# Kernel tuning notes

Hardware: AMD Instinct MI355X
Metric: run time of the kernel (lower is better)

The kernel has to match this reference:

```python
import jax, jax.numpy as jnp
import numpy as np

B, T, NH, EX, VOCAB, NLAYER = 8, 510, 12, 768, 256, 6
NBLK = 2 * NLAYER - 1          # 11 blocks, all with out=ex
NE = T + 2                     # CustomEmb output dim = n_embd = 512
HD = EX // NH
EXIT_SCALE = 1.0 / float(np.sqrt(4 * NBLK))  # torch init divides 'exit' params by sqrt(#exit params)


def _ln(x, s, b):
    m = jnp.mean(x, axis=-1, keepdims=True)
    v = jnp.mean((x - m) ** 2, axis=-1, keepdims=True)
    return (x - m) * jax.lax.rsqrt(v + 1e-5) * s + b


def setup_inputs() -> dict:
    key = jax.random.key(0)
    ks = iter(jax.random.split(key, 40))
    def n(shape, scale=0.02):
        return jax.random.normal(next(ks), shape, jnp.float32) * scale
    inp = {}
    inp['idx'] = jax.random.randint(next(ks), (B, T), 0, 2)
    inp['lin_w'] = n((NE, EX)); inp['lin_b'] = n((EX,))
    # stacked per-block params (leading dim NBLK), torch Linear math y = x @ W + b with W stored (in,out)
    inp['ln1_s'] = jnp.ones((NBLK, EX), jnp.float32); inp['ln1_b'] = jnp.zeros((NBLK, EX), jnp.float32)
    inp['qw'] = n((NBLK, EX, EX)); inp['qb'] = n((NBLK, EX))
    inp['kw'] = n((NBLK, EX, EX)); inp['kb'] = n((NBLK, EX))
    inp['vw'] = n((NBLK, EX, EX)); inp['vb'] = n((NBLK, EX))
    inp['ew'] = n((NBLK, EX, EX)) * EXIT_SCALE; inp['eb'] = n((NBLK, EX)) * EXIT_SCALE
    inp['ln2_s'] = jnp.ones((NBLK, EX), jnp.float32); inp['ln2_b'] = jnp.zeros((NBLK, EX), jnp.float32)
    inp['m1w'] = n((NBLK, EX, 4 * EX)); inp['m1b'] = n((NBLK, 4 * EX))
    inp['m2w'] = n((NBLK, 4 * EX, EX)) * EXIT_SCALE; inp['m2b'] = n((NBLK, EX)) * EXIT_SCALE
    inp['lnf_s'] = jnp.ones((EX,), jnp.float32); inp['lnf_b'] = jnp.zeros((EX,), jnp.float32)
    inp['head_w'] = n((EX * T, VOCAB)); inp['head_b'] = n((VOCAB,))
    return inp


def reference(idx, lin_w, lin_b, ln1_s, ln1_b, qw, qb, kw, kb, vw, vb, ew, eb,
              ln2_s, ln2_b, m1w, m1b, m2w, m2b, lnf_s, lnf_b, head_w, head_b):
    # CustomEmb: one-hot of binary token + identity positional encoding -> [B,T,T+2]
    e0 = (idx == 0).astype(jnp.float32)
    e1 = (idx == 1).astype(jnp.float32)
    pos = jnp.broadcast_to(jnp.eye(T, dtype=jnp.float32), (B, T, T))
    x = jnp.concatenate([e0[:, :, None], e1[:, :, None], pos], axis=2)
    x = jax.nn.relu(x @ lin_w + lin_b)                       # [B,T,EX]
    mask = jnp.tril(jnp.ones((T, T), bool))
    inv_sqrt_d = 1.0 / float(np.sqrt(HD))

    def block(x, p):
        l1s, l1b, Qw, Qb, Kw, Kb, Vw, Vb, Ew, Eb, l2s, l2b, M1w, M1b, M2w, M2b = p
        h = _ln(x, l1s, l1b)
        q = (h @ Qw + Qb).reshape(B, T, NH, HD)
        k = (h @ Kw + Kb).reshape(B, T, NH, HD)
        v = (h @ Vw + Vb).reshape(B, T, NH, HD)
        att = jnp.einsum('bqhd,bkhd->bhqk', q, k) * inv_sqrt_d
        att = jnp.where(mask, att, -jnp.inf)
        probs = jax.nn.softmax(att, axis=-1)
        y = jnp.einsum('bhqk,bkhd->bqhd', probs, v).reshape(B, T, EX)
        x = x + y @ Ew + Eb
        h2 = _ln(x, l2s, l2b)
        x = x + jax.nn.relu(h2 @ M1w + M1b) @ M2w + M2b      # MLP depth=2: initial+relu+exit
        return x, None

    x, _ = jax.lax.scan(block, x, (ln1_s, ln1_b, qw, qb, kw, kb, vw, vb,
                                   ew, eb, ln2_s, ln2_b, m1w, m1b, m2w, m2b))
    x = _ln(x, lnf_s, lnf_b)
    return x.reshape(B, -1) @ head_w + head_b                # [B, VOCAB]
```

## Files before the change

### kernel.cpp

```cpp
#include <hip/hip_runtime.h>
#include <hip/hip_bf16.h>
#include <math.h>

constexpr int cB = 8, cT = 510, cNH = 12, cEX = 768, cVOC = 256, cNBLK = 11, cHD = 64;
constexpr int cMB = 512;
constexpr int cMP = 4096;
constexpr int cQKV = 3 * cEX;

typedef __attribute__((ext_vector_type(8))) short bf16x8;
typedef __attribute__((ext_vector_type(4))) float f32x4;
using bf16 = __hip_bfloat16;

__device__ inline void gload16(const void* g, void* l) {
    __builtin_amdgcn_global_load_lds((const __attribute__((address_space(1))) unsigned int*)g,
                                     (__attribute__((address_space(3))) unsigned int*)l, 16, 0, 0);
}
__device__ inline short f2bs(float f) {
    bf16 b = __float2bfloat16(f);
    return *reinterpret_cast<short*>(&b);
}
__device__ inline float bs2f(unsigned short s) {
    unsigned int u = ((unsigned int)s) << 16;
    float f;
    __builtin_memcpy(&f, &u, 4);
    return f;
}

__global__ __launch_bounds__(256) void embed_kernel(
    const int* __restrict__ idx, const float* __restrict__ lin_w,
    const float* __restrict__ lin_b, short* __restrict__ x)
{
    int row = blockIdx.x;
    int b = row >> 9, t = row & 511;
    short* xr = x + (size_t)row * cEX;
    if (t >= cT) {
        for (int j = threadIdx.x; j < cEX; j += 256) xr[j] = 0;
        return;
    }
    int tok = idx[b * cT + t] & 1;
    const float* wt = lin_w + (size_t)tok * cEX;
    const float* wp = lin_w + (size_t)(2 + t) * cEX;
    for (int j = threadIdx.x; j < cEX; j += 256) {
        float val = wt[j] + wp[j] + lin_b[j];
        xr[j] = f2bs(fmaxf(val, 0.0f));
    }
}

__global__ __launch_bounds__(256) void ln_wave(
    const short* __restrict__ in, const float* __restrict__ s,
    const float* __restrict__ bsh, short* __restrict__ out)
{
    const int wid = threadIdx.x >> 6, lane = threadIdx.x & 63;
    const int row = blockIdx.x * 4 + wid;
    const short* xr = in + (size_t)row * cEX;
    float v[12];
    float sum = 0.f, sq = 0.f;
#pragma unroll
    for (int p = 0; p < 3; ++p) {
        ushort4 raw = *(const ushort4*)&xr[p * 256 + lane * 4];
        v[p * 4 + 0] = bs2f(raw.x); v[p * 4 + 1] = bs2f(raw.y);
        v[p * 4 + 2] = bs2f(raw.z); v[p * 4 + 3] = bs2f(raw.w);
#pragma unroll
        for (int q = 0; q < 4; ++q) { sum += v[p * 4 + q]; sq += v[p * 4 + q] * v[p * 4 + q]; }
    }
#pragma unroll
    for (int off = 1; off < 64; off <<= 1) {
        sum += __shfl_xor(sum, off, 64);
        sq  += __shfl_xor(sq, off, 64);
    }
    float mean = sum * (1.0f / cEX);
    float var = sq * (1.0f / cEX) - mean * mean;
    float rstd = rsqrtf(var + 1e-5f);
    short* outr = out + (size_t)row * cEX;
#pragma unroll
    for (int p = 0; p < 3; ++p) {
        int c = p * 256 + lane * 4;
        float4 sv = *(const float4*)&s[c];
        float4 bv = *(const float4*)&bsh[c];
        short4 pk;
        pk.x = f2bs((v[p * 4 + 0] - mean) * rstd * sv.x + bv.x);
        pk.y = f2bs((v[p * 4 + 1] - mean) * rstd * sv.y + bv.y);
        pk.z = f2bs((v[p * 4 + 2] - mean) * rstd * sv.z + bv.z);
        pk.w = f2bs((v[p * 4 + 3] - mean) * rstd * sv.w + bv.w);
        *(short4*)&outr[c] = pk;
    }
}

__global__ __launch_bounds__(256) void transpose_w(
    const float* __restrict__ W, bf16* __restrict__ WT,
    int K, int N, size_t w_stride, size_t wt_stride, int wt_row_off)
{
    __shared__ float t[32][33];
    const float* Wb = W + (size_t)blockIdx.z * w_stride;
    bf16* WTb = WT + (size_t)blockIdx.z * wt_stride;
    int n0 = blockIdx.x * 32, k0 = blockIdx.y * 32;
    int c = threadIdx.x & 31, ty = threadIdx.x >> 5;
#pragma unroll
    for (int it = 0; it < 4; ++it) {
        int r = ty + it * 8;
        t[r][c] = Wb[(size_t)(k0 + r) * N + n0 + c];
    }
    __syncthreads();
#pragma unroll
    for (int it = 0; it < 4; ++it) {
        int a = ty + it * 8;
        WTb[(size_t)(wt_row_off + n0 + a) * K + k0 + c] = __float2bfloat16(t[c][a]);
    }
}

__global__ __launch_bounds__(256) void transpose_qkv(
    const float* __restrict__ qw, const float* __restrict__ kw,
    const float* __restrict__ vw, bf16* __restrict__ WT)
{
    __shared__ float t[32][33];
    int z = blockIdx.z;
    int blk = z / 3, which = z - blk * 3;
    const float* Wb = (which == 0 ? qw : which == 1 ? kw : vw) + (size_t)blk * cEX * cEX;
    bf16* WTb = WT + (size_t)blk * cQKV * cEX + (size_t)which * cEX * cEX;
    int n0 = blockIdx.x * 32, k0 = blockIdx.y * 32;
    int c = threadIdx.x & 31, ty = threadIdx.x >> 5;
#pragma unroll
    for (int it = 0; it < 4; ++it) {
        int r = ty + it * 8;
        t[r][c] = Wb[(size_t)(k0 + r) * cEX + n0 + c];
    }
    __syncthreads();
#pragma unroll
    for (int it = 0; it < 4; ++it) {
        int a = ty + it * 8;
        WTb[(size_t)(n0 + a) * cEX + k0 + c] = __float2bfloat16(t[c][a]);
    }
}

__global__ __launch_bounds__(256) void concat_bias(
    const float* __restrict__ qb, const float* __restrict__ kb,
    const float* __restrict__ vb, float* __restrict__ qkvb)
{
    int i = blockIdx.x * 256 + threadIdx.x;
    if (i >= cNBLK * cQKV) return;
    int blk = i / cQKV, c = i - blk * cQKV;
    const float* src; int cc = c;
    if (c < cEX)            { src = qb; }
    else if (c < 2 * cEX)   { src = kb; cc = c - cEX; }
    else                    { src = vb; cc = c - 2 * cEX; }
    qkvb[i] = src[(size_t)blk * cEX + cc];
}

template<int FM, int FN, bool RELU, bool RESID, bool OUTBF16, bool VT>
__global__ __launch_bounds__(256) void gemm_db(
    const short* __restrict__ A, const short* __restrict__ BT,
    const float* __restrict__ bias, const short* __restrict__ resid,
    void* __restrict__ Cout, short* __restrict__ vTr, int K, int N)
{
    constexpr int BM = FM * 32, BN = FN * 32;
    constexpr int TS = (BM + BN) * 64;
    constexpr int CA = BM / 32, CB = BN / 32;
    constexpr int LPT = CA + CB;
    static_assert(LPT >= 5 && LPT <= 8, "vmcnt literal range");
    __shared__ short lds[2 * TS];
    const int tid = threadIdx.x;
    const int lane = tid & 63, wid = tid >> 6;
    const int wm = wid >> 1, wn = wid & 1;
    const int bm = blockIdx.y * BM, bn = blockIdx.x * BN;
    const int li = lane & 15, gk = lane >> 4;

    f32x4 acc[FM][FN];
#pragma unroll
    for (int i = 0; i < FM; ++i)
#pragma unroll
        for (int j = 0; j < FN; ++j)
            acc[i][j] = f32x4{0.f, 0.f, 0.f, 0.f};

    auto stage = [&](int kt, int buf) {
        short* la = &lds[buf * TS];
        short* lb = la + BM * 64;
#pragma unroll
        for (int i = 0; i < CA; ++i) {
            int s = i * 256 + tid;
            int r = s >> 3, c = s & 7;
            gload16(A + (size_t)(bm + r) * K + kt * 64 + (c ^ (r & 7)) * 8,
                    (char*)la + (size_t)(i * 256 + wid * 64) * 16);
        }
#pragma unroll
        for (int i = 0; i < CB; ++i) {
            int s = i * 256 + tid;
            int r = s >> 3, c = s & 7;
            gload16(BT + (size_t)(bn + r) * K + kt * 64 + (c ^ (r & 7)) * 8,
                    (char*)lb + (size_t)(i * 256 + wid * 64) * 16);
        }
    };

    const int nkt = K >> 6;
    stage(0, 0);
    stage(1, 1);

    for (int t = 0; t < nkt; ++t) {
        if (t + 1 < nkt) {
            if constexpr (LPT == 5)      asm volatile("s_waitcnt vmcnt(5)" ::: "memory");
            else if constexpr (LPT == 6) asm volatile("s_waitcnt vmcnt(6)" ::: "memory");
            else if constexpr (LPT == 7) asm volatile("s_waitcnt vmcnt(7)" ::: "memory");
            else                         asm volatile("s_waitcnt vmcnt(8)" ::: "memory");
        } else {
            asm volatile("s_waitcnt vmcnt(0)" ::: "memory");
        }
        __builtin_amdgcn_s_barrier();

        const short* la = &lds[(t & 1) * TS];
        const short* lb = la + BM * 64;

        bf16x8 af0[FM], bf0[FN];
#pragma unroll
        for (int mi = 0; mi < FM; ++mi) {
            int row = (wm * FM + mi) * 16 + li;
            af0[mi] = *(const bf16x8*)&la[row * 64 + (gk ^ (row & 7)) * 8];
        }
#pragma unroll
        for (int ni = 0; ni < FN; ++ni) {
            int row = (wn * FN + ni) * 16 + li;
            bf0[ni] = *(const bf16x8*)&lb[row * 64 + (gk ^ (row & 7)) * 8];
        }
        __builtin_amdgcn_s_setprio(1);
#pragma unroll
        for (int mi = 0; mi < FM; ++mi)
#pragma unroll
            for (int ni = 0; ni < FN; ++ni)
                acc[mi][ni] = __builtin_amdgcn_mfma_f32_16x16x32_bf16(
                    af0[mi], bf0[ni], acc[mi][ni], 0, 0, 0);
        __builtin_amdgcn_s_setprio(0);

        bf16x8 af1[FM], bf1[FN];
#pragma unroll
        for (int mi = 0; mi < FM; ++mi) {
            int row = (wm * FM + mi) * 16 + li;
            af1[mi] = *(const bf16x8*)&la[row * 64 + ((4 + gk) ^ (row & 7)) * 8];
        }
#pragma unroll
        for (int ni = 0; ni < FN; ++ni) {
            int row = (wn * FN + ni) * 16 + li;
            bf1[ni] = *(const bf16x8*)&lb[row * 64 + ((4 + gk) ^ (row & 7)) * 8];
        }
        asm volatile("s_waitcnt lgkmcnt(0)" ::: "memory");
        __builtin_amdgcn_s_barrier();
        if (t + 2 < nkt) stage(t + 2, t & 1);
        __builtin_amdgcn_s_setprio(1);
#pragma unroll
        for (int mi = 0; mi < FM; ++mi)
#pragma unroll
            for (int ni = 0; ni < FN; ++ni)
                acc[mi][ni] = __builtin_amdgcn_mfma_f32_16x16x32_bf16(
                    af1[mi], bf1[ni], acc[mi][ni], 0, 0, 0);
        __builtin_amdgcn_s_setprio(0);
    }

#pragma unroll
    for (int mi = 0; mi < FM; ++mi) {
#pragma unroll
        for (int ni = 0; ni < FN; ++ni) {
            int col = bn + (wn * FN + ni) * 16 + li;
            float bv = bias[col];
            int row0 = bm + (wm * FM + mi) * 16 + gk * 4;
            if (VT && col >= 2 * cEX) {
                short4 pk;
                pk.x = f2bs(acc[mi][ni][0] + bv);
                pk.y = f2bs(acc[mi][ni][1] + bv);
                pk.z = f2bs(acc[mi][ni][2] + bv);
                pk.w = f2bs(acc[mi][ni][3] + bv);
                *(short4*)&vTr[(size_t)(col - 2 * cEX) * cMP + row0] = pk;
            } else {
#pragma unroll
                for (int j = 0; j < 4; ++j) {
                    int row = row0 + j;
                    float v = acc[mi][ni][j] + bv;
                    if (RELU) v = fmaxf(v, 0.0f);
                    if (RESID) v += bs2f((unsigned short)resid[(size_t)row * N + col]);
                    if (OUTBF16)
                        ((bf16*)Cout)[(size_t)row * N + col] = __float2bfloat16(v);
                    else
                        ((float*)Cout)[(size_t)row * N + col] = v;
                }
            }
        }
    }
}

__global__ __launch_bounds__(256) void attn_mfma(
    const short* __restrict__ qkv, const short* __restrict__ vT, bf16* __restrict__ y)
{
    const int bid = blockIdx.x;
    const int q8 = bid & 7;
    const int j = bid >> 3;
    const int rng = bid >> 8;
    int qt;
    if (rng == 0)      qt = q8;
    else if (rng == 1) qt = 7 - q8;
    else               qt = (q8 + j) & 7;
    const int h = j % cNH, b = j / cNH;

    __shared__ short Ks[2][64 * 64];
    __shared__ short Vs[2][64 * 64];
    __shared__ short Ss[4][16][72];
    const int tid = threadIdx.x;
    const int lane = tid & 63, wid = tid >> 6;
    const int li = lane & 15, gk = lane >> 4;

    const size_t rowb = (size_t)b * cMB;
    int qr = qt * 64 + wid * 16 + li;
    int qrc = qr < cT ? qr : cT - 1;
    const short* qrow = qkv + (rowb + qrc) * cQKV + h * cHD;
    bf16x8 qf0 = *(const bf16x8*)(qrow + gk * 8);
    bf16x8 qf1 = *(const bf16x8*)(qrow + 32 + gk * 8);

    f32x4 o[4];
    float mrow[4], lrow[4];
#pragma unroll
    for (int dt = 0; dt < 4; ++dt) o[dt] = f32x4{0.f, 0.f, 0.f, 0.f};
#pragma unroll
    for (int jj = 0; jj < 4; ++jj) { mrow[jj] = -3e38f; lrow[jj] = 0.f; }

    const int qloc = qt * 64 + wid * 16 + gk * 4;

    auto stage = [&](int kt, int buf) {
#pragma unroll
        for (int i = 0; i < 2; ++i) {
            int s = i * 256 + tid;
            int r = s >> 3, c = s & 7;
            gload16(qkv + (rowb + kt * 64 + r) * cQKV + cEX + h * cHD + (c ^ (r & 7)) * 8,
                    (char*)&Ks[buf][0] + (size_t)(i * 256 + wid * 64) * 16);
        }
#pragma unroll
        for (int i = 0; i < 2; ++i) {
            int s = i * 256 + tid;
            int d = s >> 3, c = s & 7;
            gload16(vT + (size_t)(h * cHD + d) * cMP + rowb + kt * 64 + (c ^ (d & 7)) * 8,
                    (char*)&Vs[buf][0] + (size_t)(i * 256 + wid * 64) * 16);
        }
    };

    const int nkt = qt + 1;
    stage(0, 0);
    for (int kt = 0; kt < nkt; ++kt) {
        if (kt + 1 < nkt) {
            stage(kt + 1, (kt + 1) & 1);
            asm volatile("s_waitcnt vmcnt(4)" ::: "memory");
        } else {
            asm volatile("s_waitcnt vmcnt(0)" ::: "memory");
        }
        __builtin_amdgcn_s_barrier();
        const int cur = kt & 1;

        f32x4 sg[4];
#pragma unroll
        for (int g = 0; g < 4; ++g) sg[g] = f32x4{0.f, 0.f, 0.f, 0.f};
        __builtin_amdgcn_s_setprio(1);
#pragma unroll
        for (int g = 0; g < 4; ++g) {
            int key = g * 16 + li;
            bf16x8 k0 = *(const bf16x8*)&Ks[cur][key * 64 + (gk ^ (key & 7)) * 8];
            bf16x8 k1 = *(const bf16x8*)&Ks[cur][key * 64 + ((4 + gk) ^ (key & 7)) * 8];
            sg[g] = __builtin_amdgcn_mfma_f32_16x16x32_bf16(qf0, k0, sg[g], 0, 0, 0);
            sg[g] = __builtin_amdgcn_mfma_f32_16x16x32_bf16(qf1, k1, sg[g], 0, 0, 0);
        }
        __builtin_amdgcn_s_setprio(0);

#pragma unroll
        for (int jj = 0; jj < 4; ++jj) {
            int q = qloc + jj;
            float sc[4];
#pragma unroll
            for (int g = 0; g < 4; ++g) {
                int kg = kt * 64 + g * 16 + li;
                sc[g] = (kg <= q) ? sg[g][jj] * 0.125f : -3e38f;
            }
            float tm = fmaxf(fmaxf(sc[0], sc[1]), fmaxf(sc[2], sc[3]));
            tm = fmaxf(tm, __shfl_xor(tm, 1, 16));
            tm = fmaxf(tm, __shfl_xor(tm, 2, 16));
            tm = fmaxf(tm, __shfl_xor(tm, 4, 16));
            tm = fmaxf(tm, __shfl_xor(tm, 8, 16));
            float mnew = fmaxf(mrow[jj], tm);
            float p[4], ps = 0.f;
#pragma unroll
            for (int g = 0; g < 4; ++g) { p[g] = __expf(sc[g] - mnew); ps += p[g]; }
            ps += __shfl_xor(ps, 1, 16);
            ps += __shfl_xor(ps, 2, 16);
            ps += __shfl_xor(ps, 4, 16);
            ps += __shfl_xor(ps, 8, 16);
            float scale = __expf(mrow[jj] - mnew);
            lrow[jj] = lrow[jj] * scale + ps;
            mrow[jj] = mnew;
#pragma unroll
            for (int dt = 0; dt < 4; ++dt) o[dt][jj] *= scale;
#pragma unroll
            for (int g = 0; g < 4; ++g)
                Ss[wid][gk * 4 + jj][g * 16 + li] = f2bs(p[g]);
        }

        bf16x8 pa0 = *(const bf16x8*)&Ss[wid][li][gk * 8];
        bf16x8 pa1 = *(const bf16x8*)&Ss[wid][li][32 + gk * 8];
        __builtin_amdgcn_s_setprio(1);
#pragma unroll
        for (int dt = 0; dt < 4; ++dt) {
            int d = dt * 16 + li;
            bf16x8 vf0 = *(const bf16x8*)&Vs[cur][d * 64 + (gk ^ (d & 7)) * 8];
            bf16x8 vf1 = *(const bf16x8*)&Vs[cur][d * 64 + ((4 + gk) ^ (d & 7)) * 8];
            o[dt] = __builtin_amdgcn_mfma_f32_16x16x32_bf16(pa0, vf0, o[dt], 0, 0, 0);
            o[dt] = __builtin_amdgcn_mfma_f32_16x16x32_bf16(pa1, vf1, o[dt], 0, 0, 0);
        }
        __builtin_amdgcn_s_setprio(0);
        asm volatile("s_waitcnt lgkmcnt(0)" ::: "memory");
        __builtin_amdgcn_s_barrier();
    }

#pragma unroll
    for (int jj = 0; jj < 4; ++jj) {
        int q = qloc + jj;
        if (q >= cT) continue;
        float inv = 1.0f / lrow[jj];
        bf16* yr = y + (rowb + q) * cEX + h * cHD;
#pragma unroll
        for (int dt = 0; dt < 4; ++dt)
            yr[dt * 16 + li] = __float2bfloat16(o[dt][jj] * inv);
    }
}

__global__ __launch_bounds__(256) void head_part_kernel(
    const short* __restrict__ x, const float* __restrict__ lnf_s,
    const float* __restrict__ lnf_b, const float* __restrict__ hw,
    float* __restrict__ part)
{
    __shared__ float xs[8][1536];
    __shared__ float stat[16][2];
    const int tid = threadIdx.x;
    const int trow0 = blockIdx.x * 2;
    const int wid = tid >> 6, lane = tid & 63;
    {
        const int g = lane >> 4, li = lane & 15;
        const int p = wid * 4 + g, bb = p >> 1, rr = p & 1;
        const short* xr = x + ((size_t)(bb * cMB + trow0 + rr)) * cEX;
        float sum = 0.f, sq = 0.f;
#pragma unroll
        for (int it = 0; it < 12; ++it) {
            ushort4 raw = *(const ushort4*)&xr[it * 64 + li * 4];
            float a0 = bs2f(raw.x), a1 = bs2f(raw.y), a2 = bs2f(raw.z), a3 = bs2f(raw.w);
            sum += a0 + a1 + a2 + a3;
            sq  += a0 * a0 + a1 * a1 + a2 * a2 + a3 * a3;
        }
#pragma unroll
        for (int off = 8; off > 0; off >>= 1) {
            sum += __shfl_xor(sum, off, 16);
            sq  += __shfl_xor(sq, off, 16);
        }
        if (li == 0) {
            float mean = sum * (1.0f / cEX);
            float var = sq * (1.0f / cEX) - mean * mean;
            stat[p][0] = mean;
            stat[p][1] = rsqrtf(var + 1e-5f);
        }
    }
    __syncthreads();
    for (int i = tid; i < 8 * 1536; i += 256) {
        int bb = i / 1536, kk = i - bb * 1536;
        int rr = kk >= cEX ? 1 : 0;
        int e = kk - rr * cEX;
        float mean = stat[bb * 2 + rr][0], rstd = stat[bb * 2 + rr][1];
        float val = bs2f((unsigned short)x[((size_t)(bb * cMB + trow0 + rr)) * cEX + e]);
        xs[bb][kk] = (val - mean) * rstd * lnf_s[e] + lnf_b[e];
    }
    __syncthreads();
    float acc[8] = {};
    const int k0 = blockIdx.x * 1536;
    const float* wp = hw + (size_t)k0 * cVOC + tid;
    for (int kk = 0; kk < 1536; ++kk) {
        float w = wp[(size_t)kk * cVOC];
#pragma unroll
        for (int bb = 0; bb < 8; ++bb) acc[bb] += xs[bb][kk] * w;
    }
#pragma unroll
    for (int bb = 0; bb < 8; ++bb)
        part[((size_t)blockIdx.x * 8 + bb) * cVOC + tid] = acc[bb];
}

__global__ __launch_bounds__(256) void head_reduce_kernel(
    const float* __restrict__ part, const float* __restrict__ hb, float* __restrict__ out)
{
    int i = blockIdx.x * 256 + threadIdx.x;
    int bb = i >> 8, vv = i & 255;
    float acc = hb[vv];
    for (int c = 0; c < 255; ++c) acc += part[((size_t)c * 8 + bb) * 256 + vv];
    out[i] = acc;
}

extern "C" void kernel_launch(void* const* d_in, const int* in_sizes, int n_in,
                              void* d_out, int out_size, void* d_ws, size_t ws_size,
                              hipStream_t stream) {
    (void)in_sizes; (void)n_in; (void)out_size; (void)ws_size;
    const int*   idx    = (const int*)d_in[0];
    const float* lin_w  = (const float*)d_in[1];
    const float* lin_b  = (const float*)d_in[2];
    const float* ln1_s  = (const float*)d_in[3];
    const float* ln1_b  = (const float*)d_in[4];
    const float* qw     = (const float*)d_in[5];
    const float* qbias  = (const float*)d_in[6];
    const float* kw     = (const float*)d_in[7];
    const float* kbias  = (const float*)d_in[8];
    const float* vw     = (const float*)d_in[9];
    const float* vbias  = (const float*)d_in[10];
    const float* ew     = (const float*)d_in[11];
    const float* ebias  = (const float*)d_in[12];
    const float* ln2_s  = (const float*)d_in[13];
    const float* ln2_b  = (const float*)d_in[14];
    const float* m1w    = (const float*)d_in[15];
    const float* m1b    = (const float*)d_in[16];
    const float* m2w    = (const float*)d_in[17];
    const float* m2b    = (const float*)d_in[18];
    const float* lnf_s  = (const float*)d_in[19];
    const float* lnf_b  = (const float*)d_in[20];
    const float* head_w = (const float*)d_in[21];
    const float* head_b = (const float*)d_in[22];
    float* out = (float*)d_out;

    const size_t act = (size_t)cMP * cEX;
    float* part = (float*)d_ws;
    float* qkvb = part + 255 * 8 * 256;
    short* x    = (short*)(qkvb + cNBLK * cQKV);
    short* qkv  = x + act;
    short* vTr  = qkv + (size_t)cMP * cQKV;
    short* h    = vTr + (size_t)cEX * cMP;
    short* h2   = h + act;
    short* y    = h2 + act;
    short* u    = y + act;
    short* wqkvT = u + (size_t)cMP * 4 * cEX;
    short* weT   = wqkvT + (size_t)cNBLK * cQKV * cEX;
    short* wm1T  = weT + (size_t)cNBLK * cEX * cEX;
    short* wm2T  = wm1T + (size_t)cNBLK * cEX * 4 * cEX;

    transpose_qkv<<<dim3(24, 24, 3 * cNBLK), 256, 0, stream>>>(qw, kw, vw, (bf16*)wqkvT);
    transpose_w<<<dim3(24, 24, cNBLK), 256, 0, stream>>>(ew, (bf16*)weT, cEX, cEX,
        (size_t)cEX * cEX, (size_t)cEX * cEX, 0);
    transpose_w<<<dim3(96, 24, cNBLK), 256, 0, stream>>>(m1w, (bf16*)wm1T, cEX, 4 * cEX,
        (size_t)cEX * 4 * cEX, (size_t)cEX * 4 * cEX, 0);
    transpose_w<<<dim3(24, 96, cNBLK), 256, 0, stream>>>(m2w, (bf16*)wm2T, 4 * cEX, cEX,
        (size_t)cEX * 4 * cEX, (size_t)cEX * 4 * cEX, 0);
    concat_bias<<<(cNBLK * cQKV + 255) / 256, 256, 0, stream>>>(qbias, kbias, vbias, qkvb);

    embed_kernel<<<cMP, 256, 0, stream>>>(idx, lin_w, lin_b, x);

    for (int blk = 0; blk < cNBLK; ++blk) {
        size_t bo = (size_t)blk * cEX;
        ln_wave<<<cMP / 4, 256, 0, stream>>>(x, ln1_s + bo, ln1_b + bo, h);
        gemm_db<4, 3, false, false, true, true><<<dim3(cQKV / 96, cMP / 128), 256, 0, stream>>>(
            h, wqkvT + (size_t)blk * cQKV * cEX, qkvb + (size_t)blk * cQKV, nullptr,
            qkv, vTr, cEX, cQKV);
        attn_mfma<<<8 * cNH * cB, 256, 0, stream>>>(qkv, vTr, (bf16*)y);
        gemm_db<2, 3, false, true, true, false><<<dim3(cEX / 96, cMP / 64), 256, 0, stream>>>(
            y, weT + (size_t)blk * cEX * cEX, ebias + bo, x, x, nullptr, cEX, cEX);
        ln_wave<<<cMP / 4, 256, 0, stream>>>(x, ln2_s + bo, ln2_b + bo, h2);
        gemm_db<4, 4, true, false, true, false><<<dim3(4 * cEX / 128, cMP / 128), 256, 0, stream>>>(
            h2, wm1T + (size_t)blk * cEX * 4 * cEX, m1b + (size_t)blk * 4 * cEX, nullptr,
            u, nullptr, cEX, 4 * cEX);
        gemm_db<2, 3, false, true, true, false><<<dim3(cEX / 96, cMP / 64), 256, 0, stream>>>(
            u, wm2T + (size_t)blk * cEX * 4 * cEX, m2b + bo, x, x, nullptr, 4 * cEX, cEX);
    }
    head_part_kernel<<<255, 256, 0, stream>>>(x, lnf_s, lnf_b, head_w, part);
    head_reduce_kernel<<<8, 256, 0, stream>>>(part, head_b, out);
}
```

Measured before the change: 1.672 ms.

## Fold LayerNorm into following GEMMs using per-row stats from residual epilogues

Removes the standalone LayerNorm kernels. The LN scale is folded into the transposed QKV and MLP1 weights. The mean/rstd correction is applied in the GEMM epilogue using precomputed column sums (c1) and a bias term that includes the LN shift times W (cc). Per-row sum and sum-of-squares partials are emitted by the residual GEMM epilogues and the embedding, then reduced in the consumer GEMM prologue and the head kernel. This saves two activation read/write passes and two launches per block, at the cost of extra setup kernels, epilogue shuffles, and numerical risk from the single-pass variance and applying LN after the bf16 matmul.

```diff
diff --git a/kernel.cpp b/kernel.cpp
--- a/kernel.cpp
+++ b/kernel.cpp
@@ -28,77 +28,62 @@
 
 __global__ __launch_bounds__(256) void embed_kernel(
     const int* __restrict__ idx, const float* __restrict__ lin_w,
-    const float* __restrict__ lin_b, short* __restrict__ x)
+    const float* __restrict__ lin_b, short* __restrict__ x, float* __restrict__ pstat)
 {
     int row = blockIdx.x;
     int b = row >> 9, t = row & 511;
     short* xr = x + (size_t)row * cEX;
+    const int tid = threadIdx.x;
+    float s1 = 0.f, s2 = 0.f;
     if (t >= cT) {
-        for (int j = threadIdx.x; j < cEX; j += 256) xr[j] = 0;
-        return;
-    }
-    int tok = idx[b * cT + t] & 1;
-    const float* wt = lin_w + (size_t)tok * cEX;
-    const float* wp = lin_w + (size_t)(2 + t) * cEX;
-    for (int j = threadIdx.x; j < cEX; j += 256) {
-        float val = wt[j] + wp[j] + lin_b[j];
-        xr[j] = f2bs(fmaxf(val, 0.0f));
-    }
-}
-
-__global__ __launch_bounds__(256) void ln_wave(
-    const short* __restrict__ in, const float* __restrict__ s,
-    const float* __restrict__ bsh, short* __restrict__ out)
-{
-    const int wid = threadIdx.x >> 6, lane = threadIdx.x & 63;
-    const int row = blockIdx.x * 4 + wid;
-    const short* xr = in + (size_t)row * cEX;
-    float v[12];
-    float sum = 0.f, sq = 0.f;
-#pragma unroll
-    for (int p = 0; p < 3; ++p) {
-        ushort4 raw = *(const ushort4*)&xr[p * 256 + lane * 4];
-        v[p * 4 + 0] = bs2f(raw.x); v[p * 4 + 1] = bs2f(raw.y);
-        v[p * 4 + 2] = bs2f(raw.z); v[p * 4 + 3] = bs2f(raw.w);
-#pragma unroll
-        for (int q = 0; q < 4; ++q) { sum += v[p * 4 + q]; sq += v[p * 4 + q] * v[p * 4 + q]; }
+        for (int j = tid; j < cEX; j += 256) xr[j] = 0;
+    } else {
+        int tok = idx[b * cT + t] & 1;
+        const float* wt = lin_w + (size_t)tok * cEX;
+        const float* wp = lin_w + (size_t)(2 + t) * cEX;
+        for (int j = tid; j < cEX; j += 256) {
+            float val = fmaxf(wt[j] + wp[j] + lin_b[j], 0.0f);
+            short sv = f2bs(val);
+            xr[j] = sv;
+            float vr = bs2f((unsigned short)sv);
+            s1 += vr; s2 += vr * vr;
+        }
     }
 #pragma unroll
     for (int off = 1; off < 64; off <<= 1) {
-        sum += __shfl_xor(sum, off, 64);
-        sq  += __shfl_xor(sq, off, 64);
-    }
-    float mean = sum * (1.0f / cEX);
-    float var = sq * (1.0f / cEX) - mean * mean;
-    float rstd = rsqrtf(var + 1e-5f);
-    short* outr = out + (size_t)row * cEX;
-#pragma unroll
-    for (int p = 0; p < 3; ++p) {
-        int c = p * 256 + lane * 4;
-        float4 sv = *(const float4*)&s[c];
-        float4 bv = *(const float4*)&bsh[c];
-        short4 pk;
-        pk.x = f2bs((v[p * 4 + 0] - mean) * rstd * sv.x + bv.x);
-        pk.y = f2bs((v[p * 4 + 1] - mean) * rstd * sv.y + bv.y);
-        pk.z = f2bs((v[p * 4 + 2] - mean) * rstd * sv.z + bv.z);
-        pk.w = f2bs((v[p * 4 + 3] - mean) * rstd * sv.w + bv.w);
-        *(short4*)&outr[c] = pk;
+        s1 += __shfl_xor(s1, off, 64);
+        s2 += __shfl_xor(s2, off, 64);
+    }
+    __shared__ float ss[4][2];
+    int w = tid >> 6;
+    if ((tid & 63) == 0) { ss[w][0] = s1; ss[w][1] = s2; }
+    __syncthreads();
+    if (tid == 0) {
+        pstat[(size_t)row * 2 + 0] = ss[0][0] + ss[1][0] + ss[2][0] + ss[3][0];
+        pstat[(size_t)row * 2 + 1] = ss[0][1] + ss[1][1] + ss[2][1] + ss[3][1];
+    }
+    if (tid >= 1 && tid < 8) {
+        pstat[((size_t)tid * cMP + row) * 2 + 0] = 0.f;
+        pstat[((size_t)tid * cMP + row) * 2 + 1] = 0.f;
     }
 }
 
 __global__ __launch_bounds__(256) void transpose_w(
-    const float* __restrict__ W, bf16* __restrict__ WT,
+    const float* __restrict__ W, const float* __restrict__ scale, bf16* __restrict__ WT,
     int K, int N, size_t w_stride, size_t wt_stride, int wt_row_off)
 {
     __shared__ float t[32][33];
     const float* Wb = W + (size_t)blockIdx.z * w_stride;
+    const float* sb = scale ? scale + (size_t)blockIdx.z * cEX : nullptr;
     bf16* WTb = WT + (size_t)blockIdx.z * wt_stride;
     int n0 = blockIdx.x * 32, k0 = blockIdx.y * 32;
     int c = threadIdx.x & 31, ty = threadIdx.x >> 5;
 #pragma unroll
     for (int it = 0; it < 4; ++it) {
         int r = ty + it * 8;
-        t[r][c] = Wb[(size_t)(k0 + r) * N + n0 + c];
+        float v = Wb[(size_t)(k0 + r) * N + n0 + c];
+        if (scale) v *= sb[k0 + r];
+        t[r][c] = v;
     }
     __syncthreads();
 #pragma unroll
@@ -110,19 +95,20 @@
 
 __global__ __launch_bounds__(256) void transpose_qkv(
     const float* __restrict__ qw, const float* __restrict__ kw,
-    const float* __restrict__ vw, bf16* __restrict__ WT)
+    const float* __restrict__ vw, const float* __restrict__ ln1_s, bf16* __restrict__ WT)
 {
     __shared__ float t[32][33];
     int z = blockIdx.z;
     int blk = z / 3, which = z - blk * 3;
     const float* Wb = (which == 0 ? qw : which == 1 ? kw : vw) + (size_t)blk * cEX * cEX;
+    const float* sb = ln1_s + (size_t)blk * cEX;
     bf16* WTb = WT + (size_t)blk * cQKV * cEX + (size_t)which * cEX * cEX;
     int n0 = blockIdx.x * 32, k0 = blockIdx.y * 32;
     int c = threadIdx.x & 31, ty = threadIdx.x >> 5;
 #pragma unroll
     for (int it = 0; it < 4; ++it) {
         int r = ty + it * 8;
-        t[r][c] = Wb[(size_t)(k0 + r) * cEX + n0 + c];
+        t[r][c] = Wb[(size_t)(k0 + r) * cEX + n0 + c] * sb[k0 + r];
     }
     __syncthreads();
 #pragma unroll
@@ -132,25 +118,44 @@
     }
 }
 
-__global__ __launch_bounds__(256) void concat_bias(
-    const float* __restrict__ qb, const float* __restrict__ kb,
-    const float* __restrict__ vb, float* __restrict__ qkvb)
-{
-    int i = blockIdx.x * 256 + threadIdx.x;
-    if (i >= cNBLK * cQKV) return;
-    int blk = i / cQKV, c = i - blk * cQKV;
-    const float* src; int cc = c;
-    if (c < cEX)            { src = qb; }
-    else if (c < 2 * cEX)   { src = kb; cc = c - cEX; }
-    else                    { src = vb; cc = c - 2 * cEX; }
-    qkvb[i] = src[(size_t)blk * cEX + cc];
-}
-
-template<int FM, int FN, bool RELU, bool RESID, bool OUTBF16, bool VT>
+__global__ __launch_bounds__(256) void rowsum_c1(
+    const short* __restrict__ WT, float* __restrict__ c1)
+{
+    const int w = threadIdx.x >> 6, lane = threadIdx.x & 63;
+    const size_t row = (size_t)blockIdx.x * 4 + w;
+    const short* rp = WT + row * cEX;
+    float s = 0.f;
+#pragma unroll
+    for (int i = 0; i < 3; ++i) {
+        ushort4 raw = *(const ushort4*)&rp[i * 256 + lane * 4];
+        s += bs2f(raw.x) + bs2f(raw.y) + bs2f(raw.z) + bs2f(raw.w);
+    }
+#pragma unroll
+    for (int off = 1; off < 64; off <<= 1) s += __shfl_xor(s, off, 64);
+    if (lane == 0) c1[row] = s;
+}
+
+__global__ __launch_bounds__(256) void c2comp(
+    const float* __restrict__ W, const float* __restrict__ bvec,
+    const float* __restrict__ bias, float* __restrict__ cc,
+    int K, int N, int cc_stride, int co)
+{
+    int blk = blockIdx.y;
+    int n = blockIdx.x * 256 + threadIdx.x;
+    const float* Wb = W + (size_t)blk * K * N;
+    const float* bb = bvec + (size_t)blk * K;
+    float acc = bias[(size_t)blk * N + n];
+    for (int k = 0; k < K; ++k) acc += bb[k] * Wb[(size_t)k * N + n];
+    cc[(size_t)blk * cc_stride + co + n] = acc;
+}
+
+template<int FM, int FN, bool RELU, bool RESID, bool OUTBF16, bool VT, bool STATS, bool LNC>
 __global__ __launch_bounds__(256) void gemm_db(
     const short* __restrict__ A, const short* __restrict__ BT,
     const float* __restrict__ bias, const short* __restrict__ resid,
-    void* __restrict__ Cout, short* __restrict__ vTr, int K, int N)
+    void* __restrict__ Cout, short* __restrict__ vTr,
+    float* __restrict__ pstat, const float* __restrict__ c1,
+    const float* __restrict__ cc, int K, int N)
 {
     constexpr int BM = FM * 32, BN = FN * 32;
     constexpr int TS = (BM + BN) * 64;
@@ -158,6 +163,7 @@
     constexpr int LPT = CA + CB;
     static_assert(LPT >= 5 && LPT <= 8, "vmcnt literal range");
     __shared__ short lds[2 * TS];
+    __shared__ float sstat[BM][2];
     const int tid = threadIdx.x;
     const int lane = tid & 63, wid = tid >> 6;
     const int wm = wid >> 1, wn = wid & 1;
@@ -193,6 +199,21 @@
     const int nkt = K >> 6;
     stage(0, 0);
     stage(1, 1);
+
+    if (LNC) {
+        for (int r = tid; r < BM; r += 256) {
+            float a = 0.f, b2 = 0.f;
+#pragma unroll
+            for (int cb = 0; cb < 8; ++cb) {
+                a  += pstat[((size_t)cb * cMP + bm + r) * 2 + 0];
+                b2 += pstat[((size_t)cb * cMP + bm + r) * 2 + 1];
+            }
+            float mean = a * (1.0f / cEX);
+            float var = b2 * (1.0f / cEX) - mean * mean;
+            sstat[r][0] = mean;
+            sstat[r][1] = rsqrtf(var + 1e-5f);
+        }
+    }
 
     for (int t = 0; t < nkt; ++t) {
         if (t + 1 < nkt) {
@@ -252,33 +273,86 @@
         __builtin_amdgcn_s_setprio(0);
     }
 
+    float s1l[FM][4], s2l[FM][4];
+    if (STATS) {
+#pragma unroll
+        for (int mi = 0; mi < FM; ++mi)
+#pragma unroll
+            for (int j = 0; j < 4; ++j) { s1l[mi][j] = 0.f; s2l[mi][j] = 0.f; }
+    }
 #pragma unroll
     for (int mi = 0; mi < FM; ++mi) {
 #pragma unroll
         for (int ni = 0; ni < FN; ++ni) {
             int col = bn + (wn * FN + ni) * 16 + li;
-            float bv = bias[col];
             int row0 = bm + (wm * FM + mi) * 16 + gk * 4;
+            float c1v = 0.f, ccv = 0.f, bv = 0.f;
+            if (LNC) { c1v = c1[col]; ccv = cc[col]; }
+            else     { bv = bias[col]; }
             if (VT && col >= 2 * cEX) {
                 short4 pk;
-                pk.x = f2bs(acc[mi][ni][0] + bv);
-                pk.y = f2bs(acc[mi][ni][1] + bv);
-                pk.z = f2bs(acc[mi][ni][2] + bv);
-                pk.w = f2bs(acc[mi][ni][3] + bv);
+#pragma unroll
+                for (int j = 0; j < 4; ++j) {
+                    int rl = (wm * FM + mi) * 16 + gk * 4 + j;
+                    float v = LNC ? (sstat[rl][1] * acc[mi][ni][j]
+                                     - sstat[rl][1] * sstat[rl][0] * c1v + ccv)
+                                  : (acc[mi][ni][j] + bv);
+                    ((short*)&pk)[j] = f2bs(v);
+                }
                 *(short4*)&vTr[(size_t)(col - 2 * cEX) * cMP + row0] = pk;
             } else {
 #pragma unroll
                 for (int j = 0; j < 4; ++j) {
+                    int rl = (wm * FM + mi) * 16 + gk * 4 + j;
                     int row = row0 + j;
-                    float v = acc[mi][ni][j] + bv;
+                    float v;
+                    if (LNC) v = sstat[rl][1] * acc[mi][ni][j]
+                                 - sstat[rl][1] * sstat[rl][0] * c1v + ccv;
+                    else     v = acc[mi][ni][j] + bv;
                     if (RELU) v = fmaxf(v, 0.0f);
                     if (RESID) v += bs2f((unsigned short)resid[(size_t)row * N + col]);
-                    if (OUTBF16)
-                        ((bf16*)Cout)[(size_t)row * N + col] = __float2bfloat16(v);
-                    else
+                    if (OUTBF16) {
+                        short sv = f2bs(v);
+                        ((bf16*)Cout)[(size_t)row * N + col] = *reinterpret_cast<bf16*>(&sv);
+                        if (STATS) {
+                            float vr = bs2f((unsigned short)sv);
+                            s1l[mi][j] += vr; s2l[mi][j] += vr * vr;
+                        }
+                    } else {
                         ((float*)Cout)[(size_t)row * N + col] = v;
+                    }
                 }
             }
+        }
+    }
+    if (STATS) {
+#pragma unroll
+        for (int mi = 0; mi < FM; ++mi)
+#pragma unroll
+            for (int j = 0; j < 4; ++j) {
+#pragma unroll
+                for (int off = 1; off < 16; off <<= 1) {
+                    s1l[mi][j] += __shfl_xor(s1l[mi][j], off, 16);
+                    s2l[mi][j] += __shfl_xor(s2l[mi][j], off, 16);
+                }
+            }
+        float* sred = (float*)lds;
+        if (li == 0) {
+#pragma unroll
+            for (int mi = 0; mi < FM; ++mi)
+#pragma unroll
+                for (int j = 0; j < 4; ++j) {
+                    int rl = (wm * FM + mi) * 16 + gk * 4 + j;
+                    sred[(wn * BM + rl) * 2 + 0] = s1l[mi][j];
+                    sred[(wn * BM + rl) * 2 + 1] = s2l[mi][j];
+                }
+        }
+        __syncthreads();
+        if (tid < BM) {
+            float p1 = sred[tid * 2 + 0] + sred[(BM + tid) * 2 + 0];
+            float p2 = sred[tid * 2 + 1] + sred[(BM + tid) * 2 + 1];
+            pstat[((size_t)blockIdx.x * cMP + bm + tid) * 2 + 0] = p1;
+            pstat[((size_t)blockIdx.x * cMP + bm + tid) * 2 + 1] = p2;
         }
     }
 }
@@ -423,38 +497,27 @@
 }
 
 __global__ __launch_bounds__(256) void head_part_kernel(
-    const short* __restrict__ x, const float* __restrict__ lnf_s,
-    const float* __restrict__ lnf_b, const float* __restrict__ hw,
-    float* __restrict__ part)
+    const short* __restrict__ x, const float* __restrict__ pstat,
+    const float* __restrict__ lnf_s, const float* __restrict__ lnf_b,
+    const float* __restrict__ hw, float* __restrict__ part)
 {
     __shared__ float xs[8][1536];
     __shared__ float stat[16][2];
     const int tid = threadIdx.x;
     const int trow0 = blockIdx.x * 2;
-    const int wid = tid >> 6, lane = tid & 63;
-    {
-        const int g = lane >> 4, li = lane & 15;
-        const int p = wid * 4 + g, bb = p >> 1, rr = p & 1;
-        const short* xr = x + ((size_t)(bb * cMB + trow0 + rr)) * cEX;
-        float sum = 0.f, sq = 0.f;
-#pragma unroll
-        for (int it = 0; it < 12; ++it) {
-            ushort4 raw = *(const ushort4*)&xr[it * 64 + li * 4];
-            float a0 = bs2f(raw.x), a1 = bs2f(raw.y), a2 = bs2f(raw.z), a3 = bs2f(raw.w);
-            sum += a0 + a1 + a2 + a3;
-            sq  += a0 * a0 + a1 * a1 + a2 * a2 + a3 * a3;
-        }
-#pragma unroll
-        for (int off = 8; off > 0; off >>= 1) {
-            sum += __shfl_xor(sum, off, 16);
-            sq  += __shfl_xor(sq, off, 16);
-        }
-        if (li == 0) {
-            float mean = sum * (1.0f / cEX);
-            float var = sq * (1.0f / cEX) - mean * mean;
-            stat[p][0] = mean;
-            stat[p][1] = rsqrtf(var + 1e-5f);
-        }
+    if (tid < 16) {
+        int bb = tid >> 1, rr = tid & 1;
+        int row = bb * cMB + trow0 + rr;
+        float a = 0.f, b2 = 0.f;
+#pragma unroll
+        for (int cb = 0; cb < 8; ++cb) {
+            a  += pstat[((size_t)cb * cMP + row) * 2 + 0];
+            b2 += pstat[((size_t)cb * cMP + row) * 2 + 1];
+        }
+        float mean = a * (1.0f / cEX);
+        float var = b2 * (1.0f / cEX) - mean * mean;
+        stat[tid][0] = mean;
+        stat[tid][1] = rsqrtf(var + 1e-5f);
     }
     __syncthreads();
     for (int i = tid; i < 8 * 1536; i += 256) {
@@ -519,47 +582,58 @@
     float* out = (float*)d_out;
 
     const size_t act = (size_t)cMP * cEX;
-    float* part = (float*)d_ws;
-    float* qkvb = part + 255 * 8 * 256;
-    short* x    = (short*)(qkvb + cNBLK * cQKV);
-    short* qkv  = x + act;
-    short* vTr  = qkv + (size_t)cMP * cQKV;
-    short* h    = vTr + (size_t)cEX * cMP;
-    short* h2   = h + act;
-    short* y    = h2 + act;
-    short* u    = y + act;
+    float* part  = (float*)d_ws;
+    float* pstat = part + 522240;
+    float* c1q   = pstat + 65536;
+    float* ccq   = c1q + cNBLK * cQKV;
+    float* c1m   = ccq + cNBLK * cQKV;
+    float* ccm   = c1m + cNBLK * 4 * cEX;
+    short* x     = (short*)(ccm + cNBLK * 4 * cEX);
+    short* qkv   = x + act;
+    short* vTr   = qkv + (size_t)cMP * cQKV;
+    short* y     = vTr + (size_t)cEX * cMP;
+    short* u     = y + act;
     short* wqkvT = u + (size_t)cMP * 4 * cEX;
     short* weT   = wqkvT + (size_t)cNBLK * cQKV * cEX;
     short* wm1T  = weT + (size_t)cNBLK * cEX * cEX;
     short* wm2T  = wm1T + (size_t)cNBLK * cEX * 4 * cEX;
 
-    transpose_qkv<<<dim3(24, 24, 3 * cNBLK), 256, 0, stream>>>(qw, kw, vw, (bf16*)wqkvT);
-    transpose_w<<<dim3(24, 24, cNBLK), 256, 0, stream>>>(ew, (bf16*)weT, cEX, cEX,
+    transpose_qkv<<<dim3(24, 24, 3 * cNBLK), 256, 0, stream>>>(qw, kw, vw, ln1_s, (bf16*)wqkvT);
+    transpose_w<<<dim3(24, 24, cNBLK), 256, 0, stream>>>(ew, nullptr, (bf16*)weT, cEX, cEX,
         (size_t)cEX * cEX, (size_t)cEX * cEX, 0);
-    transpose_w<<<dim3(96, 24, cNBLK), 256, 0, stream>>>(m1w, (bf16*)wm1T, cEX, 4 * cEX,
+    transpose_w<<<dim3(96, 24, cNBLK), 256, 0, stream>>>(m1w, ln2_s, (bf16*)wm1T, cEX, 4 * cEX,
         (size_t)cEX * 4 * cEX, (size_t)cEX * 4 * cEX, 0);
-    transpose_w<<<dim3(24, 96, cNBLK), 256, 0, stream>>>(m2w, (bf16*)wm2T, 4 * cEX, cEX,
+    transpose_w<<<dim3(24, 96, cNBLK), 256, 0, stream>>>(m2w, nullptr, (bf16*)wm2T, 4 * cEX, cEX,
         (size_t)cEX * 4 * cEX, (size_t)cEX * 4 * cEX, 0);
-    concat_bias<<<(cNBLK * cQKV + 255) / 256, 256, 0, stream>>>(qbias, kbias, vbias, qkvb);
-
-    embed_kernel<<<cMP, 256, 0, stream>>>(idx, lin_w, lin_b, x);
+    rowsum_c1<<<cNBLK * cQKV / 4, 256, 0, stream>>>(wqkvT, c1q);
+    rowsum_c1<<<cNBLK * 4 * cEX / 4, 256, 0, stream>>>(wm1T, c1m);
+    c2comp<<<dim3(3, cNBLK), 256, 0, stream>>>(qw, ln1_b, qbias, ccq, cEX, cEX, cQKV, 0);
+    c2comp<<<dim3(3, cNBLK), 256, 0, stream>>>(kw, ln1_b, kbias, ccq, cEX, cEX, cQKV, cEX);
+    c2comp<<<dim3(3, cNBLK), 256, 0, stream>>>(vw, ln1_b, vbias, ccq, cEX, cEX, cQKV, 2 * cEX);
+    c2comp<<<dim3(12, cNBLK), 256, 0, stream>>>(m1w, ln2_b, m1b, ccm, cEX, 4 * cEX, 4 * cEX, 0);
+
+    embed_kernel<<<cMP, 256, 0, stream>>>(idx, lin_w, lin_b, x, pstat);
 
     for (int blk = 0; blk < cNBLK; ++blk) {
         size_t bo = (size_t)blk * cEX;
-        ln_wave<<<cMP / 4, 256, 0, stream>>>(x, ln1_s + bo, ln1_b + bo, h);
-        gemm_db<4, 3, false, false, true, true><<<dim3(cQKV / 96, cMP / 128), 256, 0, stream>>>(
-            h, wqkvT + (size_t)blk * cQKV * cEX, qkvb + (size_t)blk * cQKV, nullptr,
-            qkv, vTr, cEX, cQKV);
+        gemm_db<4, 3, false, false, true, true, false, true>
+            <<<dim3(cQKV / 96, cMP / 128), 256, 0, stream>>>(
+            x, wqkvT + (size_t)blk * cQKV * cEX, nullptr, nullptr, qkv, vTr,
+            pstat, c1q + (size_t)blk * cQKV, ccq + (size_t)blk * cQKV, cEX, cQKV);
         attn_mfma<<<8 * cNH * cB, 256, 0, stream>>>(qkv, vTr, (bf16*)y);
-        gemm_db<2, 3, false, true, true, false><<<dim3(cEX / 96, cMP / 64), 256, 0, stream>>>(
-            y, weT + (size_t)blk * cEX * cEX, ebias + bo, x, x, nullptr, cEX, cEX);
-        ln_wave<<<cMP / 4, 256, 0, stream>>>(x, ln2_s + bo, ln2_b + bo, h2);
-        gemm_db<4, 4, true, false, true, false><<<dim3(4 * cEX / 128, cMP / 128), 256, 0, stream>>>(
-            h2, wm1T + (size_t)blk * cEX * 4 * cEX, m1b + (size_t)blk * 4 * cEX, nullptr,
-            u, nullptr, cEX, 4 * cEX);
-        gemm_db<2, 3, false, true, true, false><<<dim3(cEX / 96, cMP / 64), 256, 0, stream>>>(
-            u, wm2T + (size_t)blk * cEX * 4 * cEX, m2b + bo, x, x, nullptr, 4 * cEX, cEX);
-    }
-    head_part_kernel<<<255, 256, 0, stream>>>(x, lnf_s, lnf_b, head_w, part);
+        gemm_db<2, 3, false, true, true, false, true, false>
+            <<<dim3(cEX / 96, cMP / 64), 256, 0, stream>>>(
+            y, weT + (size_t)blk * cEX * cEX, ebias + bo, x, x, nullptr,
+            pstat, nullptr, nullptr, cEX, cEX);
+        gemm_db<4, 4, true, false, true, false, false, true>
+            <<<dim3(4 * cEX / 128, cMP / 128), 256, 0, stream>>>(
+            x, wm1T + (size_t)blk * cEX * 4 * cEX, nullptr, nullptr, u, nullptr,
+            pstat, c1m + (size_t)blk * 4 * cEX, ccm + (size_t)blk * 4 * cEX, cEX, 4 * cEX);
+        gemm_db<2, 3, false, true, true, false, true, false>
+            <<<dim3(cEX / 96, cMP / 64), 256, 0, stream>>>(
+            u, wm2T + (size_t)blk * cEX * 4 * cEX, m2b + bo, x, x, nullptr,
+            pstat, nullptr, nullptr, 4 * cEX, cEX);
+    }
+    head_part_kernel<<<255, 256, 0, stream>>>(x, pstat, lnf_s, lnf_b, head_w, part);
     head_reduce_kernel<<<8, 256, 0, stream>>>(part, head_b, out);
 }
```

After: 3.076 ms. +84.0%, slower.
